# Optimization experiments

Hardware: AMD Instinct MI355X
Metric: run time of the kernel (lower is better)

Reference implementation:

```python
import jax, jax.numpy as jnp
import numpy as np
from jax import lax

G, CPG, KS, N = 8, 8, 3, 9  # groups, channels per group, kernel size, ks*ks


def conv2d(x, w, b=None, pad=1):
    y = lax.conv_general_dilated(x, w, (1, 1), [(pad, pad), (pad, pad)],
                                 dimension_numbers=('NCHW', 'OIHW', 'NCHW'))
    if b is not None:
        y = y + b[None, :, None, None]
    return y


def deform_group(x, f, pw, pb, mw, mb, cw):
    # x: sampled feature (anchor slice), f: offset source (motion slice); both (b,c,h,w)
    b, c, h, w = x.shape
    offset = conv2d(f, pw, pb)                      # (b, 2N, h, w)
    m = jax.nn.sigmoid(conv2d(f, mw, mb))           # (b, N, h, w) modulation
    off = jnp.transpose(offset, (0, 2, 3, 1))       # (b, h, w, 2N): first N rows(x), last N cols(y)
    rng = jnp.arange(-1, 2, dtype=x.dtype)
    pn_x = jnp.repeat(rng, KS)                      # kernel row offset, n = kr*3 + kc
    pn_y = jnp.tile(rng, KS)                        # kernel col offset
    p0_x = jnp.arange(1, h + 1, dtype=x.dtype)[:, None, None]  # base grid starts at 1 (padding=0 here)
    p0_y = jnp.arange(1, w + 1, dtype=x.dtype)[None, :, None]
    px = p0_x + pn_x + off[..., :N]                 # (b, h, w, N)
    py = p0_y + pn_y + off[..., N:]
    fx = jnp.floor(lax.stop_gradient(px))           # p.detach().floor() in the original
    fy = jnp.floor(lax.stop_gradient(py))
    qx_lt = jnp.clip(fx, 0, h - 1)
    qx_rb = jnp.clip(fx + 1, 0, h - 1)
    qy_lt = jnp.clip(fy, 0, w - 1)
    qy_rb = jnp.clip(fy + 1, 0, w - 1)
    px = jnp.clip(px, 0, h - 1)
    py = jnp.clip(py, 0, w - 1)
    g_lt = (1 + (qx_lt - px)) * (1 + (qy_lt - py))
    g_rb = (1 - (qx_rb - px)) * (1 - (qy_rb - py))
    g_lb = (1 + (qx_lt - px)) * (1 - (qy_rb - py))
    g_rt = (1 - (qx_rb - px)) * (1 + (qy_lt - py))
    x_flat = x.reshape(b, c, h * w)

    def gather(ix, iy):
        idx = (ix * w + iy).astype(jnp.int32).reshape(b, 1, -1)  # (b,1,h*w*N)
        return jnp.take_along_axis(x_flat, idx, axis=2).reshape(b, c, h, w, N)

    x_off = (g_lt[:, None] * gather(qx_lt, qy_lt) + g_rb[:, None] * gather(qx_rb, qy_rb)
             + g_lb[:, None] * gather(qx_lt, qy_rb) + g_rt[:, None] * gather(qx_rb, qy_lt))
    x_off = x_off * jnp.transpose(m, (0, 2, 3, 1))[:, None]      # apply modulation mask
    # fused equivalent of reshape to (b,c,h*3,w*3) + conv(k=3, stride=3, no bias)
    return jnp.einsum('bchwn,ocn->bohw', x_off, cw.reshape(cw.shape[0], c, N))


def reference(o, anchor, pw, pb, mw, mb, cw, w1, b1, w2, b2):
    b, C, h, w = anchor.shape
    xg = anchor.reshape(b, G, CPG, h, w).transpose(1, 0, 2, 3, 4)  # (G,b,c,h,w)
    fg = o.reshape(b, G, CPG, h, w).transpose(1, 0, 2, 3, 4)
    tg = jax.vmap(deform_group)(xg, fg, pw, pb, mw, mb, cw)        # (G,b,c,h,w)
    target = tg.transpose(1, 0, 2, 3, 4).reshape(b, C, h, w)
    target_ = jnp.concatenate([target, anchor], axis=1)            # (b,128,h,w)
    return target + conv2d(conv2d(target_, w1, b1), w2, b2)


def setup_inputs() -> dict:
    key = jax.random.key(0)
    ks = jax.random.split(key, 11)
    B, C, H, W = 4, 64, 128, 128
    return {
        'o': jax.random.normal(ks[0], (B, C, H, W), jnp.float32),
        'anchor': jax.random.normal(ks[1], (B, C, H, W), jnp.float32),
        'pw': jax.random.normal(ks[2], (G, 2 * N, CPG, 3, 3), jnp.float32) * 0.05,
        'pb': jax.random.normal(ks[3], (G, 2 * N), jnp.float32) * 0.05,
        'mw': jax.random.normal(ks[4], (G, N, CPG, 3, 3), jnp.float32) * 0.05,
        'mb': jax.random.normal(ks[5], (G, N), jnp.float32) * 0.05,
        'cw': jax.random.normal(ks[6], (G, CPG, CPG, 3, 3), jnp.float32) * 0.05,
        'w1': jax.random.normal(ks[7], (64, 128, 3, 3), jnp.float32) * 0.05,
        'b1': jax.random.normal(ks[8], (64,), jnp.float32) * 0.05,
        'w2': jax.random.normal(ks[9], (64, 64, 3, 3), jnp.float32) * 0.05,
        'b2': jax.random.normal(ks[10], (64,), jnp.float32) * 0.05,
    }
```

## Files before the change

kernel.cpp:

```cpp
#include <hip/hip_runtime.h>


typedef __attribute__((ext_vector_type(8))) short short8;
typedef __attribute__((ext_vector_type(4))) float float4v;

#define MFMA_B16(a, b, c) __builtin_amdgcn_mfma_f32_16x16x32_bf16(a, b, c, 0, 0, 0)

__device__ __forceinline__ ushort f2bf(float f) {
    union { float f; unsigned u; } v; v.f = f;
    unsigned r = v.u + 0x7FFFu + ((v.u >> 16) & 1u);
    return (ushort)(r >> 16);
}
__device__ __forceinline__ float bf2f(ushort h) {
    union { unsigned u; float f; } v; v.u = ((unsigned)h) << 16;
    return v.f;
}

__device__ __forceinline__ void tap_wo(int gy, int gx, int n,
                                       float ox, float oy, float mzv,
                                       float* W, int* O)
{
    int ky = n / 3, kx = n - ky * 3;
    float pxf = (float)(gy + ky) + ox;
    float pyf = (float)(gx + kx) + oy;
    float fx = floorf(pxf), fy = floorf(pyf);
    float qxl = fminf(fmaxf(fx, 0.f), 127.f);
    float qxr = fminf(fmaxf(fx + 1.f, 0.f), 127.f);
    float qyl = fminf(fmaxf(fy, 0.f), 127.f);
    float qyr = fminf(fmaxf(fy + 1.f, 0.f), 127.f);
    float pxc = fminf(fmaxf(pxf, 0.f), 127.f);
    float pyc = fminf(fmaxf(pyf, 0.f), 127.f);
    float glx = 1.f + (qxl - pxc), grx = 1.f - (qxr - pxc);
    float gly = 1.f + (qyl - pyc), gry = 1.f - (qyr - pyc);
    float mm = 1.f / (1.f + __expf(-mzv));
    W[0] = glx * gly * mm; W[1] = grx * gry * mm;
    W[2] = glx * gry * mm; W[3] = grx * gly * mm;
    int ixl = (int)qxl, ixr = (int)qxr, iyl = (int)qyl, iyr = (int)qyr;
    O[0] = ixl * 128 + iyl; O[1] = ixr * 128 + iyr;
    O[2] = ixl * 128 + iyr; O[3] = ixr * 128 + iyl;
}

__device__ __forceinline__ short8 interp4(const float* W, const short8* cv)
{
    short8 out;
    #pragma unroll
    for (int ic = 0; ic < 8; ++ic) {
        float v = W[0] * bf2f((ushort)cv[0][ic]) + W[1] * bf2f((ushort)cv[1][ic])
                + W[2] * bf2f((ushort)cv[2][ic]) + W[3] * bf2f((ushort)cv[3][ic]);
        out[ic] = (short)f2bf(v);
    }
    return out;
}

__global__ __launch_bounds__(256) void prep(
    const float* __restrict__ anchor,
    const float* __restrict__ w1, const float* __restrict__ w2,
    const float* __restrict__ pw, const float* __restrict__ pb,
    const float* __restrict__ mw, const float* __restrict__ mb,
    const float* __restrict__ cw,
    ushort* __restrict__ anc_g,
    ushort* __restrict__ rw1, ushort* __restrict__ rw2,
    ushort* __restrict__ rpwh, ushort* __restrict__ rpwl,
    ushort* __restrict__ rcw)
{
    const int blk = blockIdx.x;
    if (blk < 256) {
        int pix = (blk & 63) * 256 + threadIdx.x;
        int b = blk >> 6;
        ushort tmp[64];
        #pragma unroll
        for (int ch = 0; ch < 64; ++ch)
            tmp[ch] = f2bf(anchor[(((size_t)(b * 64 + ch)) << 14) + pix]);
        #pragma unroll
        for (int grp = 0; grp < 8; ++grp) {
            short8 v;
            #pragma unroll
            for (int j = 0; j < 8; ++j) v[j] = (short)tmp[grp * 8 + j];
            *(short8*)(anc_g + ((size_t)(b * 8 + grp)) * 131072 + (size_t)pix * 8) = v;
        }
        return;
    }
    int i = (blk - 256) * 256 + threadIdx.x;
    if (i < 73728) {
        int ic = i & 127, r = i >> 7, oc = r & 63, s = r >> 6;
        rw1[i] = f2bf(w1[(oc * 128 + ic) * 9 + s]);
    }
    if (i < 36864) {
        int ic = i & 63, r = i >> 6, oc = r & 63, s = r >> 6;
        rw2[i] = f2bf(w2[(oc * 64 + ic) * 9 + s]);
    }
    if (i < 24576) {
        int k = i % 96, r = i / 96, n = r & 31, g = r >> 5;
        float v = 0.f;
        if (k < 72) {
            int s = k >> 3, ic = k & 7;
            if (n < 18)      v = pw[((g * 18 + n) * 8 + ic) * 9 + s];
            else if (n < 27) v = mw[((g * 9 + (n - 18)) * 8 + ic) * 9 + s];
        } else if (k == 72) {
            if (n < 18)      v = pb[g * 18 + n];
            else if (n < 27) v = mb[g * 9 + (n - 18)];
        }
        ushort h = f2bf(v);
        rpwh[i] = h;
        rpwl[i] = f2bf(v - bf2f(h));
    }
    if (i < 12288) {
        int k = i % 96, r = i / 96, oc = r & 15, g = r >> 4;
        float v = 0.f;
        if (k < 72 && oc < 8) {
            int n = k >> 3, ic = k & 7;
            v = cw[((g * 8 + oc) * 8 + ic) * 9 + n];
        }
        rcw[i] = f2bf(v);
    }
}

__global__ __launch_bounds__(256, 4) void deform_mfma(
    const float* __restrict__ o, const ushort* __restrict__ anc_g,
    const ushort* __restrict__ rpwh, const ushort* __restrict__ rpwl,
    const ushort* __restrict__ rcw,
    ushort* __restrict__ xcat_g, float* __restrict__ target)
{
    const int tile = blockIdx.x, g = blockIdx.y, b = blockIdx.z;
    const int ty0 = (tile >> 3) * 16, tx0 = (tile & 7) * 16;
    const int tid = threadIdx.x, lane = tid & 63, wave = tid >> 6;
    const int l15 = lane & 15, quad = lane >> 4;

    __shared__ __align__(16) ushort sU[19008];
    ushort* slabh = sU;
    ushort* slabl = sU + 2592;
    float*  sOff  = (float*)((char*)sU + 10368);
    float*  sEp   = (float*)sU;

    for (int idx = tid; idx < 8 * 324; idx += 256) {
        int ic = idx / 324; int pix = idx - ic * 324;
        int r = pix / 18, c = pix - r * 18;
        int gy = ty0 + r - 1, gx = tx0 + c - 1;
        float v = 0.f;
        if ((unsigned)gy < 128u && (unsigned)gx < 128u)
            v = o[(((size_t)(b * 64 + g * 8 + ic)) << 14) + (gy << 7) + gx];
        ushort h = f2bf(v);
        slabh[pix * 8 + ic] = h;
        slabl[pix * 8 + ic] = f2bf(v - bf2f(h));
    }
    __syncthreads();

    float4v offacc[4][2] = {};
    #pragma unroll
    for (int ks = 0; ks < 3; ++ks) {
        short8 Bh[2], Bl[2];
        #pragma unroll
        for (int nf = 0; nf < 2; ++nf) {
            int off = (g * 32 + nf * 16 + l15) * 96 + ks * 32 + quad * 8;
            Bh[nf] = *(const short8*)(rpwh + off);
            Bl[nf] = *(const short8*)(rpwl + off);
        }
        short8 Ah[4], Al[4];
        if (ks < 2) {
            int s = ks * 4 + quad, sy = s / 3, sx = s - sy * 3;
            #pragma unroll
            for (int py = 0; py < 4; ++py) {
                int row = wave * 4 + py;
                int sl = ((row + sy) * 18 + l15 + sx) * 8;
                Ah[py] = *(const short8*)(&slabh[sl]);
                Al[py] = *(const short8*)(&slabl[sl]);
            }
        } else {
            #pragma unroll
            for (int py = 0; py < 4; ++py) {
                short8 zh = {0, 0, 0, 0, 0, 0, 0, 0};
                short8 zl = {0, 0, 0, 0, 0, 0, 0, 0};
                if (quad == 0) {
                    int row = wave * 4 + py;
                    int sl = ((row + 2) * 18 + l15 + 2) * 8;
                    zh = *(const short8*)(&slabh[sl]);
                    zl = *(const short8*)(&slabl[sl]);
                } else if (quad == 1) {
                    zh[0] = (short)0x3F80;
                }
                Ah[py] = zh; Al[py] = zl;
            }
        }
        #pragma unroll
        for (int py = 0; py < 4; ++py)
            #pragma unroll
            for (int nf = 0; nf < 2; ++nf) {
                offacc[py][nf] = MFMA_B16(Ah[py], Bh[nf], offacc[py][nf]);
                offacc[py][nf] = MFMA_B16(Ah[py], Bl[nf], offacc[py][nf]);
                offacc[py][nf] = MFMA_B16(Al[py], Bh[nf], offacc[py][nf]);
            }
    }
    #pragma unroll
    for (int py = 0; py < 4; ++py) {
        int p0 = (wave * 4 + py) * 16 + quad * 4;
        #pragma unroll
        for (int nf = 0; nf < 2; ++nf) {
            int ch = nf * 16 + l15;
            if (ch < 27) {
                #pragma unroll
                for (int reg = 0; reg < 4; ++reg)
                    sOff[(p0 + reg) * 27 + ch] = offacc[py][nf][reg];
            }
        }
    }

    short8 Bw[3];
    #pragma unroll
    for (int ks = 0; ks < 3; ++ks)
        Bw[ks] = *(const short8*)(rcw + ((g * 16 + l15) * 96 + ks * 32 + quad * 8));

    const ushort* gb = anc_g + ((size_t)(b * 8 + g)) * 131072;
    const int n1 = quad, n2 = quad + 4;
    float4v cacc[4] = {};
    #pragma unroll
    for (int py = 0; py < 4; ++py) {
        int prow = wave * 4 + py;
        int p = prow * 16 + l15;
        int gy = ty0 + prow, gx = tx0 + l15;

        float W[8]; int O[8];
        tap_wo(gy, gx, n1, sOff[p * 27 + n1], sOff[p * 27 + 9 + n1],
               sOff[p * 27 + 18 + n1], &W[0], &O[0]);
        tap_wo(gy, gx, n2, sOff[p * 27 + n2], sOff[p * 27 + 9 + n2],
               sOff[p * 27 + 18 + n2], &W[4], &O[4]);
        short8 cv[8];
        #pragma unroll
        for (int j = 0; j < 8; ++j)
            cv[j] = *(const short8*)(gb + (size_t)O[j] * 8);
        short8 A0 = interp4(&W[0], &cv[0]);
        short8 A1 = interp4(&W[4], &cv[4]);
        short8 A2 = {0, 0, 0, 0, 0, 0, 0, 0};
        if (quad == 0) {
            float W2[4]; int O2[4];
            tap_wo(gy, gx, 8, sOff[p * 27 + 8], sOff[p * 27 + 17],
                   sOff[p * 27 + 26], W2, O2);
            short8 c2[4];
            #pragma unroll
            for (int j = 0; j < 4; ++j)
                c2[j] = *(const short8*)(gb + (size_t)O2[j] * 8);
            A2 = interp4(W2, c2);
        }
        cacc[py] = MFMA_B16(A0, Bw[0], cacc[py]);
        cacc[py] = MFMA_B16(A1, Bw[1], cacc[py]);
        cacc[py] = MFMA_B16(A2, Bw[2], cacc[py]);
    }

    __syncthreads();
    #pragma unroll
    for (int py = 0; py < 4; ++py) {
        if (l15 < 8) {
            #pragma unroll
            for (int reg = 0; reg < 4; ++reg)
                sEp[((wave * 4 + py) * 16 + quad * 4 + reg) * 8 + l15] = cacc[py][reg];
        }
    }
    __syncthreads();
    {
        const int p = tid;
        const int gy = ty0 + (p >> 4), gx = tx0 + (p & 15);
        float res[8];
        #pragma unroll
        for (int oc = 0; oc < 8; ++oc) res[oc] = sEp[p * 8 + oc];
        short8 pk;
        #pragma unroll
        for (int oc = 0; oc < 8; ++oc) pk[oc] = (short)f2bf(res[oc]);
        *(short8*)(xcat_g + ((size_t)(b * 8 + g)) * 131072
                   + (size_t)((gy << 7) + gx) * 8) = pk;
        #pragma unroll
        for (int oc = 0; oc < 8; ++oc)
            target[(((size_t)(b * 64 + g * 8 + oc)) << 14) + (gy << 7) + gx] = res[oc];
    }
}

__global__ __launch_bounds__(256, 2) void conv1_mfma(
    const ushort* __restrict__ xg, const ushort* __restrict__ ag,
    const ushort* __restrict__ rw1, const float* __restrict__ b1,
    ushort* __restrict__ t1)
{
    const int patch = blockIdx.x, b = blockIdx.y;
    const int px0 = (patch & 7) * 16, py0 = (patch >> 3) * 8;
    const int tid = threadIdx.x, lane = tid & 63, wave = tid >> 6;
    const int mhalf = wave & 1, nhalf = wave >> 1;
    const int l15 = lane & 15, quad = lane >> 4;

    __shared__ __align__(16) ushort sA[180 * 136];

    short8 Bc[9][2];
    #pragma unroll
    for (int s = 0; s < 9; ++s)
        #pragma unroll
        for (int nf = 0; nf < 2; ++nf) {
            int oc = nhalf * 32 + nf * 16 + l15;
            Bc[s][nf] = *(const short8*)(rw1 + ((s * 64 + oc) * 128 + quad * 8));
        }

    for (int task = tid; task < 2880; task += 256) {
        int grp = task / 180, pix = task - grp * 180;
        int r = pix / 18, c = pix - r * 18;
        int gy = py0 + r - 1, gx = px0 + c - 1;
        short8 v = {0, 0, 0, 0, 0, 0, 0, 0};
        if ((unsigned)gy < 128u && (unsigned)gx < 128u) {
            const ushort* plane = ((grp < 8) ? xg : ag)
                                  + ((size_t)(b * 8 + (grp & 7))) * 131072;
            v = *(const short8*)(plane + (size_t)((gy << 7) + gx) * 8);
        }
        *(short8*)(&sA[pix * 136 + grp * 8]) = v;
    }
    __syncthreads();

    float4v acc[4][2] = {};
    #pragma unroll
    for (int ks = 0; ks < 4; ++ks) {
        short8 Bn[9][2];
        if (ks < 3) {
            #pragma unroll
            for (int s = 0; s < 9; ++s)
                #pragma unroll
                for (int nf = 0; nf < 2; ++nf) {
                    int oc = nhalf * 32 + nf * 16 + l15;
                    Bn[s][nf] = *(const short8*)(rw1 + ((s * 64 + oc) * 128 + (ks + 1) * 32 + quad * 8));
                }
        }
        #pragma unroll
        for (int r = 0; r < 6; ++r) {
            int slabrow = mhalf * 4 + r;
            short8 A[3];
            #pragma unroll
            for (int kx = 0; kx < 3; ++kx)
                A[kx] = *(const short8*)(&sA[(slabrow * 18 + l15 + kx) * 136 + ks * 32 + quad * 8]);
            #pragma unroll
            for (int ky = 0; ky < 3; ++ky) {
                int py = r - ky;
                if (py >= 0 && py < 4) {
                    #pragma unroll
                    for (int kx = 0; kx < 3; ++kx)
                        #pragma unroll
                        for (int nf = 0; nf < 2; ++nf)
                            acc[py][nf] = MFMA_B16(A[kx], Bc[ky * 3 + kx][nf], acc[py][nf]);
                }
            }
        }
        if (ks < 3) {
            #pragma unroll
            for (int s = 0; s < 9; ++s)
                #pragma unroll
                for (int nf = 0; nf < 2; ++nf) Bc[s][nf] = Bn[s][nf];
        }
    }
    const size_t nbase = ((size_t)b) << 20;
    #pragma unroll
    for (int nf = 0; nf < 2; ++nf) {
        int oc = nhalf * 32 + nf * 16 + l15;
        float bias = b1[oc];
        #pragma unroll
        for (int py = 0; py < 4; ++py) {
            int gy = py0 + mhalf * 4 + py;
            #pragma unroll
            for (int reg = 0; reg < 4; ++reg) {
                int gx = px0 + quad * 4 + reg;
                t1[nbase + (size_t)(gy * 128 + gx) * 64 + oc] = f2bf(acc[py][nf][reg] + bias);
            }
        }
    }
}

__global__ __launch_bounds__(256, 2) void conv2_mfma(
    const ushort* __restrict__ t1, const ushort* __restrict__ rw2,
    const float* __restrict__ b2, float* outres)
{
    const int patch = blockIdx.x, b = blockIdx.y;
    const int px0 = (patch & 7) * 16, py0 = (patch >> 3) * 8;
    const int tid = threadIdx.x, lane = tid & 63, wave = tid >> 6;
    const int ohalf = wave & 1, rhalf = wave >> 1;
    const int l15 = lane & 15, quad = lane >> 4;

    __shared__ __align__(16) ushort sX[180 * 72];

    short8 Ac[9][2];
    #pragma unroll
    for (int s = 0; s < 9; ++s)
        #pragma unroll
        for (int mf = 0; mf < 2; ++mf) {
            int oc = ohalf * 32 + mf * 16 + l15;
            Ac[s][mf] = *(const short8*)(rw2 + ((s * 64 + oc) * 64 + quad * 8));
        }

    const size_t nbase = ((size_t)b) << 20;
    for (int task = tid; task < 1440; task += 256) {
        int pix = task >> 3, grp = task & 7;
        int r = pix / 18, c = pix - r * 18;
        int gy = py0 + r - 1, gx = px0 + c - 1;
        short8 v = {0, 0, 0, 0, 0, 0, 0, 0};
        if ((unsigned)gy < 128u && (unsigned)gx < 128u)
            v = *(const short8*)(t1 + nbase + (size_t)(gy * 128 + gx) * 64 + grp * 8);
        *(short8*)(&sX[pix * 72 + grp * 8]) = v;
    }
    __syncthreads();

    float4v acc[2][4] = {};
    #pragma unroll
    for (int ks = 0; ks < 2; ++ks) {
        short8 An[9][2];
        if (ks < 1) {
            #pragma unroll
            for (int s = 0; s < 9; ++s)
                #pragma unroll
                for (int mf = 0; mf < 2; ++mf) {
                    int oc = ohalf * 32 + mf * 16 + l15;
                    An[s][mf] = *(const short8*)(rw2 + ((s * 64 + oc) * 64 + 32 + quad * 8));
                }
        }
        #pragma unroll
        for (int r = 0; r < 6; ++r) {
            int slabrow = rhalf * 4 + r;
            short8 Bx[3];
            #pragma unroll
            for (int kx = 0; kx < 3; ++kx)
                Bx[kx] = *(const short8*)(&sX[(slabrow * 18 + l15 + kx) * 72 + ks * 32 + quad * 8]);
            #pragma unroll
            for (int ky = 0; ky < 3; ++ky) {
                int py = r - ky;
                if (py >= 0 && py < 4) {
                    #pragma unroll
                    for (int kx = 0; kx < 3; ++kx)
                        #pragma unroll
                        for (int mf = 0; mf < 2; ++mf)
                            acc[mf][py] = MFMA_B16(Ac[ky * 3 + kx][mf], Bx[kx], acc[mf][py]);
                }
            }
        }
        if (ks < 1) {
            #pragma unroll
            for (int s = 0; s < 9; ++s)
                #pragma unroll
                for (int mf = 0; mf < 2; ++mf) Ac[s][mf] = An[s][mf];
        }
    }
    #pragma unroll
    for (int mf = 0; mf < 2; ++mf)
        #pragma unroll
        for (int reg = 0; reg < 4; ++reg) {
            int oc = ohalf * 32 + mf * 16 + quad * 4 + reg;
            float bias = b2[oc];
            #pragma unroll
            for (int py = 0; py < 4; ++py) {
                int gy = py0 + rhalf * 4 + py, gx = px0 + l15;
                size_t idx = (((size_t)(b * 64 + oc)) << 14) + gy * 128 + gx;
                outres[idx] = acc[mf][py][reg] + bias + outres[idx];
            }
        }
}

extern "C" void kernel_launch(void* const* d_in, const int* in_sizes, int n_in,
                              void* d_out, int out_size, void* d_ws, size_t ws_size,
                              hipStream_t stream) {
    const float* o      = (const float*)d_in[0];
    const float* anchor = (const float*)d_in[1];
    const float* pw     = (const float*)d_in[2];
    const float* pb     = (const float*)d_in[3];
    const float* mw     = (const float*)d_in[4];
    const float* mb     = (const float*)d_in[5];
    const float* cw     = (const float*)d_in[6];
    const float* w1     = (const float*)d_in[7];
    const float* b1     = (const float*)d_in[8];
    const float* w2     = (const float*)d_in[9];
    const float* b2     = (const float*)d_in[10];
    float* out = (float*)d_out;

    char* ws = (char*)d_ws;
    ushort* anc_g  = (ushort*)(ws);
    ushort* xcat_g = (ushort*)(ws + 8388608);
    ushort* t1b    = (ushort*)(ws + 16777216);
    char*   wsm    = ws + 25165824;
    ushort* rw1p   = (ushort*)(wsm);
    ushort* rw2p   = (ushort*)(wsm + 147456);
    ushort* rpwh   = (ushort*)(wsm + 147456 + 73728);
    ushort* rpwl   = (ushort*)(wsm + 147456 + 73728 + 49152);
    ushort* rcwp   = (ushort*)(wsm + 147456 + 73728 + 98304);

    prep<<<544, 256, 0, stream>>>(anchor, w1, w2, pw, pb, mw, mb, cw,
                                  anc_g, rw1p, rw2p, rpwh, rpwl, rcwp);
    deform_mfma<<<dim3(64, 8, 4), 256, 0, stream>>>(o, anc_g, rpwh, rpwl, rcwp,
                                                    xcat_g, out );
    conv1_mfma<<<dim3(128, 4), 256, 0, stream>>>(xcat_g, anc_g, rw1p, b1, t1b);
    conv2_mfma<<<dim3(128, 4), 256, 0, stream>>>(t1b, rw2p, b2, out);
}
```

Before: 181.4 us.

## Halve conv tiles, swizzle LDS, stream weights per ky, pack bf16 interpolation

After: 201.6 us. +11.1%, slower.

```diff
diff --git a/kernel.cpp b/kernel.cpp
--- a/kernel.cpp
+++ b/kernel.cpp
@@ -3,6 +3,7 @@
 
 typedef __attribute__((ext_vector_type(8))) short short8;
 typedef __attribute__((ext_vector_type(4))) float float4v;
+typedef __attribute__((ext_vector_type(2))) float float2v;
 
 #define MFMA_B16(a, b, c) __builtin_amdgcn_mfma_f32_16x16x32_bf16(a, b, c, 0, 0, 0)
 
@@ -42,14 +43,26 @@
 
 __device__ __forceinline__ short8 interp4(const float* W, const short8* cv)
 {
-    short8 out;
-    #pragma unroll
-    for (int ic = 0; ic < 8; ++ic) {
-        float v = W[0] * bf2f((ushort)cv[0][ic]) + W[1] * bf2f((ushort)cv[1][ic])
-                + W[2] * bf2f((ushort)cv[2][ic]) + W[3] * bf2f((ushort)cv[3][ic]);
-        out[ic] = (short)f2bf(v);
-    }
-    return out;
+    union U { short8 s; uint4 u; };
+    uint4 c[4];
+    #pragma unroll
+    for (int j = 0; j < 4; ++j) { U t; t.s = cv[j]; c[j] = t.u; }
+    U out;
+    #pragma unroll
+    for (int p = 0; p < 4; ++p) {
+        float2v acc = {0.f, 0.f};
+        #pragma unroll
+        for (int j = 0; j < 4; ++j) {
+            unsigned d = (&c[j].x)[p];
+            float2v cc = {__uint_as_float(d << 16),
+                          __uint_as_float(d & 0xffff0000u)};
+            float2v Wv = {W[j], W[j]};
+            acc = __builtin_elementwise_fma(cc, Wv, acc);
+        }
+        unsigned u0 = __float_as_uint(acc.x), u1 = __float_as_uint(acc.y);
+        (&out.u.x)[p] = __builtin_amdgcn_perm(u1, u0, 0x07060302u);
+    }
+    return out.s;
 }
 
 __global__ __launch_bounds__(256) void prep(
@@ -272,30 +285,21 @@
     }
 }
 
-__global__ __launch_bounds__(256, 2) void conv1_mfma(
+__global__ __launch_bounds__(256, 4) void conv1_mfma(
     const ushort* __restrict__ xg, const ushort* __restrict__ ag,
     const ushort* __restrict__ rw1, const float* __restrict__ b1,
     ushort* __restrict__ t1)
 {
     const int patch = blockIdx.x, b = blockIdx.y;
-    const int px0 = (patch & 7) * 16, py0 = (patch >> 3) * 8;
+    const int px0 = (patch & 7) * 16, py0 = (patch >> 3) * 4;
     const int tid = threadIdx.x, lane = tid & 63, wave = tid >> 6;
-    const int mhalf = wave & 1, nhalf = wave >> 1;
+    const int ohalf = wave & 1, rhalf = wave >> 1;
     const int l15 = lane & 15, quad = lane >> 4;
 
-    __shared__ __align__(16) ushort sA[180 * 136];
-
-    short8 Bc[9][2];
-    #pragma unroll
-    for (int s = 0; s < 9; ++s)
-        #pragma unroll
-        for (int nf = 0; nf < 2; ++nf) {
-            int oc = nhalf * 32 + nf * 16 + l15;
-            Bc[s][nf] = *(const short8*)(rw1 + ((s * 64 + oc) * 128 + quad * 8));
-        }
-
-    for (int task = tid; task < 2880; task += 256) {
-        int grp = task / 180, pix = task - grp * 180;
+    __shared__ __align__(16) ushort sA[108 * 128];
+
+    for (int task = tid; task < 1728; task += 256) {
+        int grp = task / 108, pix = task - grp * 108;
         int r = pix / 18, c = pix - r * 18;
         int gy = py0 + r - 1, gx = px0 + c - 1;
         short8 v = {0, 0, 0, 0, 0, 0, 0, 0};
@@ -304,136 +308,107 @@
                                   + ((size_t)(b * 8 + (grp & 7))) * 131072;
             v = *(const short8*)(plane + (size_t)((gy << 7) + gx) * 8);
         }
-        *(short8*)(&sA[pix * 136 + grp * 8]) = v;
+        *(short8*)(&sA[pix * 128 + ((grp ^ (pix & 15)) * 8)]) = v;
     }
     __syncthreads();
 
-    float4v acc[4][2] = {};
+    float4v acc[2][2] = {};
     #pragma unroll
     for (int ks = 0; ks < 4; ++ks) {
-        short8 Bn[9][2];
-        if (ks < 3) {
-            #pragma unroll
-            for (int s = 0; s < 9; ++s)
+        #pragma unroll
+        for (int ky = 0; ky < 3; ++ky) {
+            short8 Bf[3][2];
+            #pragma unroll
+            for (int kx = 0; kx < 3; ++kx)
                 #pragma unroll
                 for (int nf = 0; nf < 2; ++nf) {
-                    int oc = nhalf * 32 + nf * 16 + l15;
-                    Bn[s][nf] = *(const short8*)(rw1 + ((s * 64 + oc) * 128 + (ks + 1) * 32 + quad * 8));
+                    int oc = ohalf * 32 + nf * 16 + l15;
+                    Bf[kx][nf] = *(const short8*)(rw1 +
+                        (((ky * 3 + kx) * 64 + oc) * 128 + ks * 32 + quad * 8));
                 }
-        }
-        #pragma unroll
-        for (int r = 0; r < 6; ++r) {
-            int slabrow = mhalf * 4 + r;
-            short8 A[3];
-            #pragma unroll
-            for (int kx = 0; kx < 3; ++kx)
-                A[kx] = *(const short8*)(&sA[(slabrow * 18 + l15 + kx) * 136 + ks * 32 + quad * 8]);
-            #pragma unroll
-            for (int ky = 0; ky < 3; ++ky) {
-                int py = r - ky;
-                if (py >= 0 && py < 4) {
+            #pragma unroll
+            for (int t = 0; t < 2; ++t) {
+                int row = rhalf * 2 + t + ky;
+                #pragma unroll
+                for (int kx = 0; kx < 3; ++kx) {
+                    int pix = row * 18 + l15 + kx;
+                    short8 A = *(const short8*)(&sA[pix * 128 +
+                        (((ks * 4 + quad) ^ (pix & 15)) * 8)]);
                     #pragma unroll
-                    for (int kx = 0; kx < 3; ++kx)
-                        #pragma unroll
-                        for (int nf = 0; nf < 2; ++nf)
-                            acc[py][nf] = MFMA_B16(A[kx], Bc[ky * 3 + kx][nf], acc[py][nf]);
+                    for (int nf = 0; nf < 2; ++nf)
+                        acc[t][nf] = MFMA_B16(A, Bf[kx][nf], acc[t][nf]);
                 }
             }
         }
-        if (ks < 3) {
-            #pragma unroll
-            for (int s = 0; s < 9; ++s)
-                #pragma unroll
-                for (int nf = 0; nf < 2; ++nf) Bc[s][nf] = Bn[s][nf];
-        }
     }
     const size_t nbase = ((size_t)b) << 20;
     #pragma unroll
     for (int nf = 0; nf < 2; ++nf) {
-        int oc = nhalf * 32 + nf * 16 + l15;
+        int oc = ohalf * 32 + nf * 16 + l15;
         float bias = b1[oc];
         #pragma unroll
-        for (int py = 0; py < 4; ++py) {
-            int gy = py0 + mhalf * 4 + py;
+        for (int t = 0; t < 2; ++t) {
+            int gy = py0 + rhalf * 2 + t;
             #pragma unroll
             for (int reg = 0; reg < 4; ++reg) {
                 int gx = px0 + quad * 4 + reg;
-                t1[nbase + (size_t)(gy * 128 + gx) * 64 + oc] = f2bf(acc[py][nf][reg] + bias);
-            }
-        }
-    }
-}
-
-__global__ __launch_bounds__(256, 2) void conv2_mfma(
+                t1[nbase + (size_t)((gy << 7) + gx) * 64 + oc] = f2bf(acc[t][nf][reg] + bias);
+            }
+        }
+    }
+}
+
+__global__ __launch_bounds__(256, 4) void conv2_mfma(
     const ushort* __restrict__ t1, const ushort* __restrict__ rw2,
     const float* __restrict__ b2, float* outres)
 {
     const int patch = blockIdx.x, b = blockIdx.y;
-    const int px0 = (patch & 7) * 16, py0 = (patch >> 3) * 8;
+    const int px0 = (patch & 7) * 16, py0 = (patch >> 3) * 4;
     const int tid = threadIdx.x, lane = tid & 63, wave = tid >> 6;
     const int ohalf = wave & 1, rhalf = wave >> 1;
     const int l15 = lane & 15, quad = lane >> 4;
 
-    __shared__ __align__(16) ushort sX[180 * 72];
-
-    short8 Ac[9][2];
-    #pragma unroll
-    for (int s = 0; s < 9; ++s)
-        #pragma unroll
-        for (int mf = 0; mf < 2; ++mf) {
-            int oc = ohalf * 32 + mf * 16 + l15;
-            Ac[s][mf] = *(const short8*)(rw2 + ((s * 64 + oc) * 64 + quad * 8));
-        }
+    __shared__ __align__(16) ushort sX[108 * 64];
 
     const size_t nbase = ((size_t)b) << 20;
-    for (int task = tid; task < 1440; task += 256) {
-        int pix = task >> 3, grp = task & 7;
+    for (int task = tid; task < 864; task += 256) {
+        int grp = task / 108, pix = task - grp * 108;
         int r = pix / 18, c = pix - r * 18;
         int gy = py0 + r - 1, gx = px0 + c - 1;
         short8 v = {0, 0, 0, 0, 0, 0, 0, 0};
         if ((unsigned)gy < 128u && (unsigned)gx < 128u)
-            v = *(const short8*)(t1 + nbase + (size_t)(gy * 128 + gx) * 64 + grp * 8);
-        *(short8*)(&sX[pix * 72 + grp * 8]) = v;
+            v = *(const short8*)(t1 + nbase + (size_t)((gy << 7) + gx) * 64 + grp * 8);
+        *(short8*)(&sX[pix * 64 + ((grp ^ (pix & 7)) * 8)]) = v;
     }
     __syncthreads();
 
-    float4v acc[2][4] = {};
+    float4v acc[2][2] = {};
     #pragma unroll
     for (int ks = 0; ks < 2; ++ks) {
-        short8 An[9][2];
-        if (ks < 1) {
-            #pragma unroll
-            for (int s = 0; s < 9; ++s)
+        #pragma unroll
+        for (int ky = 0; ky < 3; ++ky) {
+            short8 Aw[3][2];
+            #pragma unroll
+            for (int kx = 0; kx < 3; ++kx)
                 #pragma unroll
                 for (int mf = 0; mf < 2; ++mf) {
                     int oc = ohalf * 32 + mf * 16 + l15;
-                    An[s][mf] = *(const short8*)(rw2 + ((s * 64 + oc) * 64 + 32 + quad * 8));
+                    Aw[kx][mf] = *(const short8*)(rw2 +
+                        (((ky * 3 + kx) * 64 + oc) * 64 + ks * 32 + quad * 8));
                 }
-        }
-        #pragma unroll
-        for (int r = 0; r < 6; ++r) {
-            int slabrow = rhalf * 4 + r;
-            short8 Bx[3];
-            #pragma unroll
-            for (int kx = 0; kx < 3; ++kx)
-                Bx[kx] = *(const short8*)(&sX[(slabrow * 18 + l15 + kx) * 72 + ks * 32 + quad * 8]);
-            #pragma unroll
-            for (int ky = 0; ky < 3; ++ky) {
-                int py = r - ky;
-                if (py >= 0 && py < 4) {
+            #pragma unroll
+            for (int t = 0; t < 2; ++t) {
+                int row = rhalf * 2 + t + ky;
+                #pragma unroll
+                for (int kx = 0; kx < 3; ++kx) {
+                    int pix = row * 18 + l15 + kx;
+                    short8 Bx = *(const short8*)(&sX[pix * 64 +
+                        (((ks * 4 + quad) ^ (pix & 7)) * 8)]);
                     #pragma unroll
-                    for (int kx = 0; kx < 3; ++kx)
-                        #pragma unroll
-                        for (int mf = 0; mf < 2; ++mf)
-                            acc[mf][py] = MFMA_B16(Ac[ky * 3 + kx][mf], Bx[kx], acc[mf][py]);
+                    for (int mf = 0; mf < 2; ++mf)
+                        acc[mf][t] = MFMA_B16(Aw[kx][mf], Bx, acc[mf][t]);
                 }
             }
-        }
-        if (ks < 1) {
-            #pragma unroll
-            for (int s = 0; s < 9; ++s)
-                #pragma unroll
-                for (int mf = 0; mf < 2; ++mf) Ac[s][mf] = An[s][mf];
         }
     }
     #pragma unroll
@@ -443,10 +418,10 @@
             int oc = ohalf * 32 + mf * 16 + quad * 4 + reg;
             float bias = b2[oc];
             #pragma unroll
-            for (int py = 0; py < 4; ++py) {
-                int gy = py0 + rhalf * 4 + py, gx = px0 + l15;
-                size_t idx = (((size_t)(b * 64 + oc)) << 14) + gy * 128 + gx;
-                outres[idx] = acc[mf][py][reg] + bias + outres[idx];
+            for (int t = 0; t < 2; ++t) {
+                int gy = py0 + rhalf * 2 + t, gx = px0 + l15;
+                size_t idx = (((size_t)(b * 64 + oc)) << 14) + (gy << 7) + gx;
+                outres[idx] = acc[mf][t][reg] + bias + outres[idx];
             }
         }
 }
@@ -482,6 +457,6 @@
                                   anc_g, rw1p, rw2p, rpwh, rpwl, rcwp);
     deform_mfma<<<dim3(64, 8, 4), 256, 0, stream>>>(o, anc_g, rpwh, rpwl, rcwp,
                                                     xcat_g, out );
-    conv1_mfma<<<dim3(128, 4), 256, 0, stream>>>(xcat_g, anc_g, rw1p, b1, t1b);
-    conv2_mfma<<<dim3(128, 4), 256, 0, stream>>>(t1b, rw2p, b2, out);
-}
+    conv1_mfma<<<dim3(256, 4), 256, 0, stream>>>(xcat_g, anc_g, rw1p, b1, t1b);
+    conv2_mfma<<<dim3(256, 4), 256, 0, stream>>>(t1b, rw2p, b2, out);
+}
```
